# Kernel optimization log

Hardware: AMD Instinct MI355X
Metric: run time of the kernel (lower is better)

## Reference

```python
import jax, jax.numpy as jnp
import numpy as np

N_HEAD = 16
MASKED_BIAS = -10000.0


def setup_inputs() -> dict:
    key = jax.random.key(0)
    k1, k2, k3 = jax.random.split(key, 3)
    B, T, E = 2, 2048, 1024
    return {
        "stacked": jax.random.normal(k1, (B, T, E), dtype=jnp.float32),
        "w_attn": jax.random.normal(k2, (E, 3 * E), dtype=jnp.float32) * 0.02,
        "b_attn": jnp.zeros((3 * E,), dtype=jnp.float32),
        "w_proj": jax.random.normal(k3, (E, E), dtype=jnp.float32) * 0.02,
        "b_proj": jnp.zeros((E,), dtype=jnp.float32),
    }


def reference(stacked, w_attn, b_attn, w_proj, b_proj):
    B, T, E = stacked.shape
    nh = N_HEAD
    dh = E // nh
    # Conv1D (GPT-2): x @ W + b
    qkv = stacked @ w_attn + b_attn            # (B, T, 3E)
    q, k, v = jnp.split(qkv, 3, axis=-1)
    q = q.reshape(B, T, nh, dh).transpose(0, 2, 1, 3)  # (B, nh, T, dh)
    k = k.reshape(B, T, nh, dh).transpose(0, 2, 1, 3)
    v = v.reshape(B, T, nh, dh).transpose(0, 2, 1, 3)
    # scores = Q @ K^T / sqrt(dh)
    w = jnp.einsum("bhtd,bhsd->bhts", q, k) / jnp.sqrt(jnp.float32(dh))
    causal = jnp.tril(jnp.ones((T, T), dtype=bool))
    w = jnp.where(causal, w, jnp.float32(MASKED_BIAS))
    w = jax.nn.softmax(w, axis=-1)
    out = jnp.einsum("bhts,bhsd->bhtd", w, v)  # (B, nh, T, dh)
    out = out.transpose(0, 2, 1, 3).reshape(B, T, E)
    attn_z = out @ w_proj + b_proj
    return attn_z
```

## Files before the change

kernel.cpp:

```cpp
#include <hip/hip_runtime.h>
#include <hip/hip_bf16.h>

#define B_ 2
#define T_ 2048
#define E_ 1024
#define NH 16
#define M_ (B_*T_)
#define N3E 3072

typedef __attribute__((ext_vector_type(8))) short short8;
typedef __attribute__((ext_vector_type(4))) float f32x4;

__device__ __forceinline__ unsigned short f2bf(float f) {
  unsigned u = __builtin_bit_cast(unsigned, f);
  unsigned r = 0x7FFFu + ((u >> 16) & 1u);
  return (unsigned short)((u + r) >> 16);
}

__device__ __forceinline__ float bf2f(unsigned short s) {
  return __builtin_bit_cast(float, ((unsigned)s) << 16);
}

__device__ __forceinline__ unsigned cvtpk(float a, float b) {
  unsigned r;
  asm("v_cvt_pk_bf16_f32 %0, %1, %2" : "=v"(r) : "v"(a), "v"(b));
  return r;
}

__device__ __forceinline__ float exp2fast(float x) {
  float r;
  asm("v_exp_f32 %0, %1" : "=v"(r) : "v"(x));
  return r;
}

__device__ __forceinline__ void gload16(const void* g, void* l) {
  __builtin_amdgcn_global_load_lds(
      (const __attribute__((address_space(1))) unsigned int*)g,
      (__attribute__((address_space(3))) unsigned int*)l, 16, 0, 0);
}

__global__ void cast_kernel(const float* __restrict__ in,
                            unsigned short* __restrict__ out, int n8) {
  int i = blockIdx.x * blockDim.x + threadIdx.x;
  if (i >= n8) return;
  const float4* p = (const float4*)in + (size_t)i * 2;
  float4 a = p[0], b = p[1];
  short8 o;
  o[0] = (short)f2bf(a.x); o[1] = (short)f2bf(a.y);
  o[2] = (short)f2bf(a.z); o[3] = (short)f2bf(a.w);
  o[4] = (short)f2bf(b.x); o[5] = (short)f2bf(b.y);
  o[6] = (short)f2bf(b.z); o[7] = (short)f2bf(b.w);
  *(short8*)(out + (size_t)i * 8) = o;
}

__global__ void transpose_cast(const float* __restrict__ in,
                               unsigned short* __restrict__ out, int R, int C) {
  __shared__ float tile[32][33];
  int c0 = blockIdx.x * 32, r0 = blockIdx.y * 32;
  int tx = threadIdx.x & 31, ty = threadIdx.x >> 5;
#pragma unroll
  for (int i = 0; i < 4; i++) {
    int r = ty + i * 8;
    tile[r][tx] = in[(size_t)(r0 + r) * C + c0 + tx];
  }
  __syncthreads();
#pragma unroll
  for (int i = 0; i < 4; i++) {
    int r = ty + i * 8;
    out[(size_t)(c0 + r) * R + r0 + tx] = f2bf(tile[tx][r]);
  }
}

template <int OUTF32>
__global__ __launch_bounds__(256) void gemm_bt(
    const unsigned short* __restrict__ A, const unsigned short* __restrict__ Bt,
    const float* __restrict__ bias, void* __restrict__ outp,
    int M, int N, int K) {
  __shared__ __attribute__((aligned(16))) unsigned short Asm[128 * 32];
  __shared__ __attribute__((aligned(16))) unsigned short Bsm[128 * 32];
  const int tid = threadIdx.x;
  const int lane = tid & 63;
  const int wid = tid >> 6;
  const int wr = wid >> 1, wc = wid & 1;
  const int li = lane & 15, g = lane >> 4;
  const int bm = blockIdx.y * 128, bn = blockIdx.x * 128;

  f32x4 acc[4][4] = {};

  const int srow = tid >> 2;
  const int scol = (tid & 3) * 8;
  const unsigned short* Ag = A + (size_t)(bm + srow) * K + scol;
  const unsigned short* Bg = Bt + (size_t)(bn + srow) * K + scol;
  char* AsmB = (char*)Asm;
  char* BsmB = (char*)Bsm;
  const int ldsoff = tid * 16;

  for (int k0 = 0; k0 < K; k0 += 32) {
    __syncthreads();
    gload16(Ag + k0, AsmB + ldsoff);
    gload16(Ag + (size_t)64 * K + k0, AsmB + ldsoff + 4096);
    gload16(Bg + k0, BsmB + ldsoff);
    gload16(Bg + (size_t)64 * K + k0, BsmB + ldsoff + 4096);
    __syncthreads();
    short8 af[4], bf[4];
#pragma unroll
    for (int i = 0; i < 4; i++)
      af[i] = *(const short8*)&Asm[(wr * 64 + i * 16 + li) * 32 + g * 8];
#pragma unroll
    for (int j = 0; j < 4; j++)
      bf[j] = *(const short8*)&Bsm[(wc * 64 + j * 16 + li) * 32 + g * 8];
#pragma unroll
    for (int i = 0; i < 4; i++)
#pragma unroll
      for (int j = 0; j < 4; j++)
        acc[i][j] = __builtin_amdgcn_mfma_f32_16x16x32_bf16(af[i], bf[j],
                                                            acc[i][j], 0, 0, 0);
  }

#pragma unroll
  for (int j = 0; j < 4; j++) {
    int col = bn + wc * 64 + j * 16 + li;
    float bs = bias[col];
#pragma unroll
    for (int i = 0; i < 4; i++) {
      int row0 = bm + wr * 64 + i * 16 + g * 4;
#pragma unroll
      for (int r = 0; r < 4; r++) {
        float v = acc[i][j][r] + bs;
        if (OUTF32)
          ((float*)outp)[(size_t)(row0 + r) * N + col] = v;
        else
          ((unsigned short*)outp)[(size_t)(row0 + r) * N + col] = f2bf(v);
      }
    }
  }
}

__device__ __forceinline__ f32x4 mfma16(short8 a, short8 b, f32x4 c) {
  return __builtin_amdgcn_mfma_f32_16x16x32_bf16(a, b, c, 0, 0, 0);
}

__device__ __forceinline__ void attn_tile(
    const unsigned short* Ksm, const unsigned short* Vts,
    unsigned short (*PsmW)[72], short8 qf0, short8 qf1,
    float& m2, float& l2, f32x4* O, int qrel, bool diag, int li, int g) {
  f32x4 S[4];
  __builtin_amdgcn_s_setprio(1);
#pragma unroll
  for (int ct = 0; ct < 4; ct++) {
    int r = ct * 16 + li;
    int sw = r & 7;
    short8 k0f = *(const short8*)&Ksm[r * 64 + ((g ^ sw) << 3)];
    short8 k1f = *(const short8*)&Ksm[r * 64 + (((g + 4) ^ sw) << 3)];
    f32x4 z = {0.f, 0.f, 0.f, 0.f};
    z = mfma16(k0f, qf0, z);
    z = mfma16(k1f, qf1, z);
    S[ct] = z;
  }
  __builtin_amdgcn_s_setprio(0);

  if (diag) {
#pragma unroll
    for (int ct = 0; ct < 4; ct++)
#pragma unroll
      for (int r = 0; r < 4; r++)
        if (ct * 16 + g * 4 + r > qrel) S[ct][r] = -30000.f;
  }

  float tmax = S[0][0];
#pragma unroll
  for (int ct = 0; ct < 4; ct++)
#pragma unroll
    for (int r = 0; r < 4; r++) tmax = fmaxf(tmax, S[ct][r]);
  tmax = fmaxf(tmax, __shfl_xor(tmax, 16));
  tmax = fmaxf(tmax, __shfl_xor(tmax, 32));

  if (__any(tmax > m2 + 11.5f)) {
    float mn = fmaxf(m2, tmax);
    float cs = exp2fast(m2 - mn);
    l2 *= cs;
#pragma unroll
    for (int c2 = 0; c2 < 4; c2++)
#pragma unroll
      for (int r = 0; r < 4; r++) O[c2][r] *= cs;
    m2 = mn;
  }

  float rsum = 0.f;
#pragma unroll
  for (int ct = 0; ct < 4; ct++) {
    float p0 = exp2fast(S[ct][0] - m2);
    float p1 = exp2fast(S[ct][1] - m2);
    float p2 = exp2fast(S[ct][2] - m2);
    float p3 = exp2fast(S[ct][3] - m2);
    rsum += (p0 + p1) + (p2 + p3);
    uint2 pk;
    pk.x = cvtpk(p0, p1);
    pk.y = cvtpk(p2, p3);
    *(uint2*)&PsmW[li][ct * 16 + g * 4] = pk;
  }
  rsum += __shfl_xor(rsum, 16);
  rsum += __shfl_xor(rsum, 32);
  l2 += rsum;

  __builtin_amdgcn_s_setprio(1);
#pragma unroll
  for (int kk = 0; kk < 2; kk++) {
    short8 pf = *(const short8*)&PsmW[li][kk * 32 + g * 8];
#pragma unroll
    for (int c2 = 0; c2 < 4; c2++) {
      int d = c2 * 16 + li;
      int swd = ((d >> 3) ^ d) & 7;
      short8 vf = *(const short8*)&Vts[d * 64 + (((kk * 4 + g) ^ swd) << 3)];
      O[c2] = mfma16(vf, pf, O[c2]);
    }
  }
  __builtin_amdgcn_s_setprio(0);
}

__global__ __launch_bounds__(256) void attn_kernel(
    const unsigned short* __restrict__ qkv, unsigned short* __restrict__ aout) {
  const int pair = blockIdx.x;
  const int h = blockIdx.y, b = blockIdx.z;
  const int qa = pair, qb = (T_ / 64 - 1) - pair;
  const int tid = threadIdx.x, lane = tid & 63, w = tid >> 6;
  const int li = lane & 15, g = lane >> 4;

  __shared__ __attribute__((aligned(16))) unsigned short Ksm[2][64 * 64];
  __shared__ __attribute__((aligned(16))) unsigned short Vts[2][64 * 64];
  __shared__ __attribute__((aligned(16))) unsigned short Psm[4][16][72];

  const size_t rs = 3 * E_;
  const unsigned short* base = qkv + (size_t)b * T_ * rs + h * 64;
  const unsigned short* Kg = base + E_;
  const unsigned short* Vg = base + 2 * E_;

  const float QSC = 0.18033688f;
  short8 qfa0, qfa1, qfb0, qfb1;
  {
    const unsigned short* qrow = base + (size_t)(qa * 64 + w * 16 + li) * rs;
    short8 v0 = *(const short8*)(qrow + g * 8);
    short8 v1 = *(const short8*)(qrow + 32 + g * 8);
    qrow = base + (size_t)(qb * 64 + w * 16 + li) * rs;
    short8 v2 = *(const short8*)(qrow + g * 8);
    short8 v3 = *(const short8*)(qrow + 32 + g * 8);
#pragma unroll
    for (int j = 0; j < 8; j++) {
      qfa0[j] = (short)f2bf(bf2f((unsigned short)v0[j]) * QSC);
      qfa1[j] = (short)f2bf(bf2f((unsigned short)v1[j]) * QSC);
      qfb0[j] = (short)f2bf(bf2f((unsigned short)v2[j]) * QSC);
      qfb1[j] = (short)f2bf(bf2f((unsigned short)v3[j]) * QSC);
    }
  }

  float ma = -1e30f, la = 0.f, mb = -1e30f, lb = 0.f;
  f32x4 Oa[4] = {}, Ob[4] = {};

  short8 vreg[2];
  const int sr = tid >> 3, sch = tid & 7;

#pragma unroll
  for (int p = 0; p < 2; p++) {
    int idx = tid + p * 256;
    int r = idx >> 3, ch = idx & 7;
    int sc = (ch ^ (r & 7)) * 8;
    gload16(Kg + (size_t)r * rs + sc, (char*)&Ksm[0][0] + idx * 16);
  }
#pragma unroll
  for (int p = 0; p < 2; p++) {
    int idx = tid + p * 256;
    int r = idx >> 3, c = (idx & 7) * 8;
    vreg[p] = *(const short8*)(Vg + (size_t)r * rs + c);
  }
#pragma unroll
  for (int p = 0; p < 2; p++) {
    int idx = tid + p * 256;
    int r = idx >> 3, ch = idx & 7;
#pragma unroll
    for (int j = 0; j < 8; j++) {
      int d = ch * 8 + j;
      Vts[0][(d * 64 + r) ^ (((ch ^ j) & 7) << 3)] = (unsigned short)vreg[p][j];
    }
  }
  asm volatile("s_waitcnt vmcnt(0)" ::: "memory");
  __syncthreads();

  const int nt = qb + 1;
  for (int kv = 0; kv < nt; kv++) {
    const int cur = kv & 1, nxt = cur ^ 1;
    const bool pre = (kv + 1 < nt);
    if (pre) {
      const int s1 = (kv + 1) * 64;
#pragma unroll
      for (int p = 0; p < 2; p++) {
        int idx = tid + p * 256;
        int r = idx >> 3, c = (idx & 7) * 8;
        vreg[p] = *(const short8*)(Vg + (size_t)(s1 + r) * rs + c);
      }
#pragma unroll
      for (int p = 0; p < 2; p++) {
        int idx = tid + p * 256;
        int r = idx >> 3, ch = idx & 7;
        int sc = (ch ^ (r & 7)) * 8;
        gload16(Kg + (size_t)(s1 + r) * rs + sc,
                (char*)&Ksm[nxt][0] + idx * 16);
      }
    }

    attn_tile(&Ksm[cur][0], &Vts[cur][0], Psm[w], qfb0, qfb1, mb, lb, Ob,
              qb * 64 + w * 16 + li - kv * 64, kv == qb, li, g);
    if (kv <= qa)
      attn_tile(&Ksm[cur][0], &Vts[cur][0], Psm[w], qfa0, qfa1, ma, la, Oa,
                qa * 64 + w * 16 + li - kv * 64, kv == qa, li, g);

    if (pre) {
#pragma unroll
      for (int p = 0; p < 2; p++) {
        int idx = tid + p * 256;
        int r = idx >> 3, ch = idx & 7;
#pragma unroll
        for (int j = 0; j < 8; j++) {
          int d = ch * 8 + j;
          Vts[nxt][(d * 64 + r) ^ (((ch ^ j) & 7) << 3)] =
              (unsigned short)vreg[p][j];
        }
      }
    }
    asm volatile("s_waitcnt vmcnt(0)" ::: "memory");
    __syncthreads();
  }

  const float inva = 1.f / la, invb = 1.f / lb;
  const int rowa = b * T_ + qa * 64 + w * 16 + li;
  const int rowb = b * T_ + qb * 64 + w * 16 + li;
#pragma unroll
  for (int c2 = 0; c2 < 4; c2++) {
    uint2 oa, ob;
    oa.x = cvtpk(Oa[c2][0] * inva, Oa[c2][1] * inva);
    oa.y = cvtpk(Oa[c2][2] * inva, Oa[c2][3] * inva);
    ob.x = cvtpk(Ob[c2][0] * invb, Ob[c2][1] * invb);
    ob.y = cvtpk(Ob[c2][2] * invb, Ob[c2][3] * invb);
    *(uint2*)&aout[(size_t)rowa * E_ + h * 64 + c2 * 16 + g * 4] = oa;
    *(uint2*)&aout[(size_t)rowb * E_ + h * 64 + c2 * 16 + g * 4] = ob;
  }
  (void)sr; (void)sch;
}

extern "C" void kernel_launch(void* const* d_in, const int* in_sizes, int n_in,
                              void* d_out, int out_size, void* d_ws,
                              size_t ws_size, hipStream_t stream) {
  const float* stacked = (const float*)d_in[0];
  const float* w_attn = (const float*)d_in[1];
  const float* b_attn = (const float*)d_in[2];
  const float* w_proj = (const float*)d_in[3];
  const float* b_proj = (const float*)d_in[4];
  float* out = (float*)d_out;

  unsigned short* Abf = (unsigned short*)d_ws;
  unsigned short* WaT = Abf + (size_t)M_ * E_;
  unsigned short* WpT = WaT + (size_t)N3E * E_;
  unsigned short* qkv = WpT + (size_t)E_ * E_;
  unsigned short* aout = qkv + (size_t)M_ * N3E;

  cast_kernel<<<(M_ * E_ / 8 + 255) / 256, 256, 0, stream>>>(stacked, Abf,
                                                             M_ * E_ / 8);
  transpose_cast<<<dim3(N3E / 32, E_ / 32), 256, 0, stream>>>(w_attn, WaT, E_,
                                                              N3E);
  transpose_cast<<<dim3(E_ / 32, E_ / 32), 256, 0, stream>>>(w_proj, WpT, E_,
                                                             E_);
  gemm_bt<0><<<dim3(N3E / 128, M_ / 128), 256, 0, stream>>>(Abf, WaT, b_attn,
                                                            qkv, M_, N3E, E_);
  attn_kernel<<<dim3(T_ / 128, NH, B_), 256, 0, stream>>>(qkv, aout);
  gemm_bt<1><<<dim3(E_ / 128, M_ / 128), 256, 0, stream>>>(aout, WpT, b_proj,
                                                           out, M_, E_, E_);
}
```

Measured before the change: 130.2 us.

## Use one query tile per block and shuffle P via ds_bpermute

Each attention block now handles one 64-row query tile instead of a balanced pair (qa, T-1-qa), which doubles the grid. Heavy tiles are launched first to offset the causal imbalance. The P probabilities are also redistributed between lanes with ds_bpermute instead of being written to and re-read from a shared-memory scratch buffer, which removes the Psm array. The trade-off is that each loaded K/V tile is reused by only one query tile, so K/V global traffic per block pair roughly doubles, and per-block work becomes uneven.

```diff
diff --git a/kernel.cpp b/kernel.cpp
--- a/kernel.cpp
+++ b/kernel.cpp
@@ -10,6 +10,7 @@
 
 typedef __attribute__((ext_vector_type(8))) short short8;
 typedef __attribute__((ext_vector_type(4))) float f32x4;
+typedef __attribute__((ext_vector_type(4))) int int4v;
 
 __device__ __forceinline__ unsigned short f2bf(float f) {
   unsigned u = __builtin_bit_cast(unsigned, f);
@@ -142,8 +143,8 @@
 
 __device__ __forceinline__ void attn_tile(
     const unsigned short* Ksm, const unsigned short* Vts,
-    unsigned short (*PsmW)[72], short8 qf0, short8 qf1,
-    float& m2, float& l2, f32x4* O, int qrel, bool diag, int li, int g) {
+    short8 qf0, short8 qf1, float& m2, float& l2, f32x4* O,
+    int qrel, bool diag, int li, int g, int idx0, int idx1) {
   f32x4 S[4];
   __builtin_amdgcn_s_setprio(1);
 #pragma unroll
@@ -186,6 +187,7 @@
     m2 = mn;
   }
 
+  unsigned pkx[4], pky[4];
   float rsum = 0.f;
 #pragma unroll
   for (int ct = 0; ct < 4; ct++) {
@@ -194,19 +196,31 @@
     float p2 = exp2fast(S[ct][2] - m2);
     float p3 = exp2fast(S[ct][3] - m2);
     rsum += (p0 + p1) + (p2 + p3);
-    uint2 pk;
-    pk.x = cvtpk(p0, p1);
-    pk.y = cvtpk(p2, p3);
-    *(uint2*)&PsmW[li][ct * 16 + g * 4] = pk;
+    pkx[ct] = cvtpk(p0, p1);
+    pky[ct] = cvtpk(p2, p3);
   }
   rsum += __shfl_xor(rsum, 16);
   rsum += __shfl_xor(rsum, 32);
   l2 += rsum;
 
+  const bool hi = ((g >> 1) & 1) != 0;
   __builtin_amdgcn_s_setprio(1);
 #pragma unroll
   for (int kk = 0; kk < 2; kk++) {
-    short8 pf = *(const short8*)&PsmW[li][kk * 32 + g * 8];
+    int aXl = __builtin_amdgcn_ds_bpermute(idx0, (int)pkx[2 * kk]);
+    int aXh = __builtin_amdgcn_ds_bpermute(idx0, (int)pkx[2 * kk + 1]);
+    int aYl = __builtin_amdgcn_ds_bpermute(idx0, (int)pky[2 * kk]);
+    int aYh = __builtin_amdgcn_ds_bpermute(idx0, (int)pky[2 * kk + 1]);
+    int bXl = __builtin_amdgcn_ds_bpermute(idx1, (int)pkx[2 * kk]);
+    int bXh = __builtin_amdgcn_ds_bpermute(idx1, (int)pkx[2 * kk + 1]);
+    int bYl = __builtin_amdgcn_ds_bpermute(idx1, (int)pky[2 * kk]);
+    int bYh = __builtin_amdgcn_ds_bpermute(idx1, (int)pky[2 * kk + 1]);
+    int4v u;
+    u[0] = hi ? aXh : aXl;
+    u[1] = hi ? aYh : aYl;
+    u[2] = hi ? bXh : bXl;
+    u[3] = hi ? bYh : bYl;
+    short8 pf = __builtin_bit_cast(short8, u);
 #pragma unroll
     for (int c2 = 0; c2 < 4; c2++) {
       int d = c2 * 16 + li;
@@ -220,15 +234,13 @@
 
 __global__ __launch_bounds__(256) void attn_kernel(
     const unsigned short* __restrict__ qkv, unsigned short* __restrict__ aout) {
-  const int pair = blockIdx.x;
+  const int qt = (T_ / 64 - 1) - blockIdx.x;
   const int h = blockIdx.y, b = blockIdx.z;
-  const int qa = pair, qb = (T_ / 64 - 1) - pair;
   const int tid = threadIdx.x, lane = tid & 63, w = tid >> 6;
   const int li = lane & 15, g = lane >> 4;
 
   __shared__ __attribute__((aligned(16))) unsigned short Ksm[2][64 * 64];
   __shared__ __attribute__((aligned(16))) unsigned short Vts[2][64 * 64];
-  __shared__ __attribute__((aligned(16))) unsigned short Psm[4][16][72];
 
   const size_t rs = 3 * E_;
   const unsigned short* base = qkv + (size_t)b * T_ * rs + h * 64;
@@ -236,28 +248,25 @@
   const unsigned short* Vg = base + 2 * E_;
 
   const float QSC = 0.18033688f;
-  short8 qfa0, qfa1, qfb0, qfb1;
+  short8 qf0, qf1;
   {
-    const unsigned short* qrow = base + (size_t)(qa * 64 + w * 16 + li) * rs;
+    const unsigned short* qrow = base + (size_t)(qt * 64 + w * 16 + li) * rs;
     short8 v0 = *(const short8*)(qrow + g * 8);
     short8 v1 = *(const short8*)(qrow + 32 + g * 8);
-    qrow = base + (size_t)(qb * 64 + w * 16 + li) * rs;
-    short8 v2 = *(const short8*)(qrow + g * 8);
-    short8 v3 = *(const short8*)(qrow + 32 + g * 8);
 #pragma unroll
     for (int j = 0; j < 8; j++) {
-      qfa0[j] = (short)f2bf(bf2f((unsigned short)v0[j]) * QSC);
-      qfa1[j] = (short)f2bf(bf2f((unsigned short)v1[j]) * QSC);
-      qfb0[j] = (short)f2bf(bf2f((unsigned short)v2[j]) * QSC);
-      qfb1[j] = (short)f2bf(bf2f((unsigned short)v3[j]) * QSC);
-    }
-  }
-
-  float ma = -1e30f, la = 0.f, mb = -1e30f, lb = 0.f;
-  f32x4 Oa[4] = {}, Ob[4] = {};
+      qf0[j] = (short)f2bf(bf2f((unsigned short)v0[j]) * QSC);
+      qf1[j] = (short)f2bf(bf2f((unsigned short)v1[j]) * QSC);
+    }
+  }
+
+  const int idx0 = (li + 16 * ((2 * g) & 3)) * 4;
+  const int idx1 = (li + 16 * ((2 * g + 1) & 3)) * 4;
+
+  float m2 = -1e30f, l2 = 0.f;
+  f32x4 O[4] = {};
 
   short8 vreg[2];
-  const int sr = tid >> 3, sch = tid & 7;
 
 #pragma unroll
   for (int p = 0; p < 2; p++) {
@@ -285,7 +294,7 @@
   asm volatile("s_waitcnt vmcnt(0)" ::: "memory");
   __syncthreads();
 
-  const int nt = qb + 1;
+  const int nt = qt + 1;
   for (int kv = 0; kv < nt; kv++) {
     const int cur = kv & 1, nxt = cur ^ 1;
     const bool pre = (kv + 1 < nt);
@@ -307,11 +316,8 @@
       }
     }
 
-    attn_tile(&Ksm[cur][0], &Vts[cur][0], Psm[w], qfb0, qfb1, mb, lb, Ob,
-              qb * 64 + w * 16 + li - kv * 64, kv == qb, li, g);
-    if (kv <= qa)
-      attn_tile(&Ksm[cur][0], &Vts[cur][0], Psm[w], qfa0, qfa1, ma, la, Oa,
-                qa * 64 + w * 16 + li - kv * 64, kv == qa, li, g);
+    attn_tile(&Ksm[cur][0], &Vts[cur][0], qf0, qf1, m2, l2, O,
+              qt * 64 + w * 16 + li - kv * 64, kv == qt, li, g, idx0, idx1);
 
     if (pre) {
 #pragma unroll
@@ -330,20 +336,15 @@
     __syncthreads();
   }
 
-  const float inva = 1.f / la, invb = 1.f / lb;
-  const int rowa = b * T_ + qa * 64 + w * 16 + li;
-  const int rowb = b * T_ + qb * 64 + w * 16 + li;
+  const float inv = 1.f / l2;
+  const int row = b * T_ + qt * 64 + w * 16 + li;
 #pragma unroll
   for (int c2 = 0; c2 < 4; c2++) {
-    uint2 oa, ob;
-    oa.x = cvtpk(Oa[c2][0] * inva, Oa[c2][1] * inva);
-    oa.y = cvtpk(Oa[c2][2] * inva, Oa[c2][3] * inva);
-    ob.x = cvtpk(Ob[c2][0] * invb, Ob[c2][1] * invb);
-    ob.y = cvtpk(Ob[c2][2] * invb, Ob[c2][3] * invb);
-    *(uint2*)&aout[(size_t)rowa * E_ + h * 64 + c2 * 16 + g * 4] = oa;
-    *(uint2*)&aout[(size_t)rowb * E_ + h * 64 + c2 * 16 + g * 4] = ob;
-  }
-  (void)sr; (void)sch;
+    uint2 o;
+    o.x = cvtpk(O[c2][0] * inv, O[c2][1] * inv);
+    o.y = cvtpk(O[c2][2] * inv, O[c2][3] * inv);
+    *(uint2*)&aout[(size_t)row * E_ + h * 64 + c2 * 16 + g * 4] = o;
+  }
 }
 
 extern "C" void kernel_launch(void* const* d_in, const int* in_sizes, int n_in,
@@ -370,7 +371,7 @@
                                                              E_);
   gemm_bt<0><<<dim3(N3E / 128, M_ / 128), 256, 0, stream>>>(Abf, WaT, b_attn,
                                                             qkv, M_, N3E, E_);
-  attn_kernel<<<dim3(T_ / 128, NH, B_), 256, 0, stream>>>(qkv, aout);
+  attn_kernel<<<dim3(T_ / 64, NH, B_), 256, 0, stream>>>(qkv, aout);
   gemm_bt<1><<<dim3(E_ / 128, M_ / 128), 256, 0, stream>>>(aout, WpT, b_proj,
                                                            out, M_, E_, E_);
 }
```

Result: slower. 161.6 us (+24.1%).
